# Performance work log

Measured on AMD Instinct MI355X. Metric: run time of the kernel, lower is better.

The kernel has to match this reference:

```python
import jax, jax.numpy as jnp
import numpy as np

D_EMBED = 1024
D_HEAD = 128


def setup_inputs() -> dict:
    key = jax.random.key(0)
    kx, kq, kk, kv = jax.random.split(key, 4)
    x = jax.random.normal(kx, (4, 4096, D_EMBED), dtype=jnp.float32)
    # nn.Linear(d_embed, d_head, bias=False) weights, stored [out, in] like torch
    s = 1.0 / np.sqrt(D_EMBED)
    Wq = jax.random.uniform(kq, (D_HEAD, D_EMBED), jnp.float32, -s, s)
    Wk = jax.random.uniform(kk, (D_HEAD, D_EMBED), jnp.float32, -s, s)
    Wv = jax.random.uniform(kv, (D_HEAD, D_EMBED), jnp.float32, -s, s)
    return {"x": x, "Wq": Wq, "Wk": Wk, "Wv": Wv}


def reference(x, Wq, Wk, Wv):
    # q,k,v: [b, s, d_head]
    q = jnp.einsum("bse,he->bsh", x, Wq)
    k = jnp.einsum("bse,he->bsh", x, Wk)
    v = jnp.einsum("bse,he->bsh", x, Wv)
    # original: (q @ k^T) * d_head**-0.5, then divided by sqrt(d_embed)
    scale = 1.0 / (np.sqrt(D_HEAD) * np.sqrt(D_EMBED))
    scores = jnp.einsum("bqh,bkh->bqk", q, k) * jnp.float32(scale)  # [b, s, s]
    attn = jax.nn.softmax(scores, axis=-1)
    return jnp.einsum("bqk,bkh->bqh", attn, v)
```

## Files before the change

kernel.cpp:

```cpp
#include <hip/hip_runtime.h>
#include <stdint.h>

typedef __bf16 bf16x8 __attribute__((ext_vector_type(8)));
typedef float  f32x4  __attribute__((ext_vector_type(4)));

#define ATTN_SCALE 2.7621359e-3f

__device__ __forceinline__ unsigned short f2bf(float f) {
  union { float f; uint32_t u; } v; v.f = f;
  uint32_t u = v.u;
  uint32_t r = (u + 0x7FFFu + ((u >> 16) & 1u)) >> 16;
  return (unsigned short)r;
}

__device__ __forceinline__ void load_lds16(const unsigned short* g, unsigned short* l) {
  __builtin_amdgcn_global_load_lds(
      (const __attribute__((address_space(1))) void*)g,
      (__attribute__((address_space(3))) void*)l, 16, 0, 0);
}

__device__ __forceinline__ f32x4 mfma16(bf16x8 a, bf16x8 b, f32x4 c) {
  return __builtin_amdgcn_mfma_f32_16x16x32_bf16(a, b, c, 0, 0, 0);
}

__device__ __forceinline__ bf16x8 ones_bf16() {
  union { unsigned short u[8]; bf16x8 v; } c;
#pragma unroll
  for (int j = 0; j < 8; ++j) c.u[j] = 0x3F80;
  return c.v;
}

__global__ __launch_bounds__(256) void k_cvt(const float* __restrict__ src,
                                             unsigned short* __restrict__ dst, int n4) {
  int i = blockIdx.x * 256 + threadIdx.x;
  if (i >= n4) return;
  float4 f = ((const float4*)src)[i];
  ushort4 o;
  o.x = f2bf(f.x); o.y = f2bf(f.y); o.z = f2bf(f.z); o.w = f2bf(f.w);
  ((ushort4*)dst)[i] = o;
}

__global__ __launch_bounds__(256) void k_cvtw(const float* __restrict__ a,
                                              const float* __restrict__ b,
                                              const float* __restrict__ c,
                                              unsigned short* __restrict__ dst) {
  int i = blockIdx.x * 256 + threadIdx.x;
  int sel = i >> 15, off = i & 32767;
  const float* s = (sel == 0) ? a : (sel == 1) ? b : c;
  float4 f = ((const float4*)s)[off];
  ushort4 o;
  o.x = f2bf(f.x); o.y = f2bf(f.y); o.z = f2bf(f.z); o.w = f2bf(f.w);
  ((ushort4*)dst)[i] = o;
}

__global__ __launch_bounds__(256, 2) void k_proj(
    const unsigned short* __restrict__ X,
    const unsigned short* __restrict__ W,
    unsigned short* __restrict__ Qb,
    unsigned short* __restrict__ Kb,
    unsigned short* __restrict__ Vt)
{
  __shared__ __align__(16) unsigned short sm[128 * 32 * 2];
  unsigned short* As = sm;
  unsigned short* Bs = sm + 4096;
  const int t = threadIdx.x;
  const int mtile = blockIdx.x;
  const int nt = blockIdx.y;
  const int w = t >> 6, lane = t & 63, quad = lane >> 4, l15 = lane & 15;
  const int wm = w & 1, wn = w >> 1;

  const unsigned short* Wsel = W + nt * (128 * 1024);
  const unsigned short* Ag = X + (size_t)(mtile * 128) * 1024;

  const unsigned short* ag0 = Ag + (size_t)(t >> 2) * 1024 + (t & 3) * 8;
  const unsigned short* bg0 = Wsel + (size_t)(t >> 2) * 1024 + (t & 3) * 8;
  unsigned short* aw = &As[(t >> 6) * 512];
  unsigned short* bw = &Bs[(t >> 6) * 512];

  f32x4 acc[4][4] = {};

  for (int kt = 0; kt < 32; ++kt) {
    __syncthreads();
    const unsigned short* ak = ag0 + kt * 32;
    const unsigned short* bk = bg0 + kt * 32;
    load_lds16(ak,             aw);
    load_lds16(ak + 64 * 1024, aw + 2048);
    load_lds16(bk,             bw);
    load_lds16(bk + 64 * 1024, bw + 2048);
    __syncthreads();

    bf16x8 af[4], bfr[4];
#pragma unroll
    for (int i = 0; i < 4; ++i)
      af[i] = *(const bf16x8*)&As[(wm * 64 + i * 16 + l15) * 32 + quad * 8];
#pragma unroll
    for (int j = 0; j < 4; ++j)
      bfr[j] = *(const bf16x8*)&Bs[(wn * 64 + j * 16 + l15) * 32 + quad * 8];
#pragma unroll
    for (int i = 0; i < 4; ++i)
#pragma unroll
      for (int j = 0; j < 4; ++j)
        acc[i][j] = mfma16(af[i], bfr[j], acc[i][j]);
  }

  if (nt != 2) {
    const int m0 = mtile * 128 + wm * 64;
#pragma unroll
    for (int i = 0; i < 4; ++i)
#pragma unroll
      for (int j = 0; j < 4; ++j)
#pragma unroll
        for (int r = 0; r < 4; ++r) {
          int m = m0 + i * 16 + quad * 4 + r;
          int n = wn * 64 + j * 16 + l15;
          float v = acc[i][j][r];
          if (nt == 0) Qb[(size_t)m * 128 + n] = f2bf(v * ATTN_SCALE);
          else         Kb[(size_t)m * 128 + n] = f2bf(v);
        }
  } else {
    float* Ts = (float*)sm;
    const int bb = mtile >> 5;
    const int s0 = (mtile & 31) * 128;
#pragma unroll
    for (int jj = 0; jj < 8; ++jj) {
      __syncthreads();
      if (wn == (jj >> 2)) {
        const int j = jj & 3;
#pragma unroll
        for (int i = 0; i < 4; ++i)
#pragma unroll
          for (int r = 0; r < 4; ++r)
            Ts[(wm * 64 + i * 16 + quad * 4 + r) * 17 + l15] = acc[i][j][r];
      }
      __syncthreads();
      int n2 = jj * 16 + (t >> 4), m2 = (t & 15) * 8;
      union { unsigned short u[8]; uint4 v; } pk;
#pragma unroll
      for (int e = 0; e < 8; ++e) pk.u[e] = f2bf(Ts[(m2 + e) * 17 + (t >> 4)]);
      *(uint4*)&Vt[((size_t)(bb * 128 + n2)) * 4096 + s0 + m2] = pk.v;
    }
  }
}

__global__ __launch_bounds__(256, 2) void k_flash(
    const unsigned short* __restrict__ Qb,
    const unsigned short* __restrict__ Kb,
    const unsigned short* __restrict__ Vt,
    float* __restrict__ Om,
    float* __restrict__ lp)
{
  __shared__ __align__(16) unsigned short smem[8192 * 3 + 5120];
  unsigned short* Vsh = smem + 16384;
  unsigned short* Psh = smem + 24576;
  float* Ob  = (float*)smem;
  float* lsh = (float*)(smem + 24576);

  const int t = threadIdx.x;
  const int w = t >> 6, lane = t & 63, quad = lane >> 4, l15 = lane & 15;
  const int h = w & 1, p = w >> 1;
  const int qt = blockIdx.x, b = blockIdx.y, sp = blockIdx.z;

  const unsigned short* Qg = Qb + (size_t)(b * 4096 + qt * 64 + h * 32) * 128;
  const unsigned short* Kg = Kb + (size_t)b * 4096 * 128;
  const unsigned short* Vg = Vt + (size_t)b * 128 * 4096;

  bf16x8 qf[2][4];
#pragma unroll
  for (int mt = 0; mt < 2; ++mt)
#pragma unroll
    for (int kk = 0; kk < 4; ++kk)
      qf[mt][kk] = *(const bf16x8*)&Qg[(size_t)(mt * 16 + l15) * 128 + kk * 32 + quad * 8];

  f32x4 O[2][8] = {};
  f32x4 Ol[2] = {};

  const unsigned short* kg0 = Kg + (size_t)(t >> 4) * 128 + (((t & 15) ^ ((t >> 5) & 7)) * 8);
  const unsigned short* vg0 = Vg + (size_t)(t >> 3) * 4096 + (((t & 7) ^ ((t >> 3) & 7)) * 8);
  unsigned short* vw = &Vsh[w * 512];

  const int kt0 = sp * 32;

  {
    const unsigned short* kg = kg0 + (size_t)kt0 * 8192;
    unsigned short* kw = &smem[w * 512];
#pragma unroll
    for (int it = 0; it < 4; ++it)
      load_lds16(kg + it * 2048, kw + it * 2048);
  }

  for (int i = 0; i < 32; ++i) {
    const int cur = i & 1, nxt = cur ^ 1;
    __syncthreads();
    {
      const unsigned short* vg = vg0 + (size_t)(kt0 + i) * 64;
#pragma unroll
      for (int it = 0; it < 4; ++it)
        load_lds16(vg + (size_t)it * 131072, vw + it * 2048);
      const int ktn = (i < 31) ? (kt0 + i + 1) : kt0;
      const unsigned short* kg = kg0 + (size_t)ktn * 8192;
      unsigned short* kw = &smem[nxt * 8192 + w * 512];
#pragma unroll
      for (int it = 0; it < 4; ++it)
        load_lds16(kg + it * 2048, kw + it * 2048);
    }

    const unsigned short* Kshc = &smem[cur * 8192];
    f32x4 sc[2][2] = {};
#pragma unroll
    for (int ntk = 0; ntk < 2; ++ntk) {
      const int row = p * 32 + 2 * l15 + ntk;
#pragma unroll
      for (int kk = 0; kk < 4; ++kk) {
        bf16x8 kf = *(const bf16x8*)&Kshc[row * 128 + (((kk * 4 + quad) ^ (l15 & 7)) * 8)];
        sc[0][ntk] = mfma16(qf[0][kk], kf, sc[0][ntk]);
        sc[1][ntk] = mfma16(qf[1][kk], kf, sc[1][ntk]);
      }
    }

#pragma unroll
    for (int mt = 0; mt < 2; ++mt)
#pragma unroll
      for (int r = 0; r < 4; ++r) {
        float e0 = __expf(sc[mt][0][r]);
        float e1 = __expf(sc[mt][1][r]);
        int row = mt * 16 + quad * 4 + r;
        uint32_t pk = (uint32_t)f2bf(e0) | ((uint32_t)f2bf(e1) << 16);
        *(uint32_t*)&Psh[w * 1280 + row * 40 + 2 * l15] = pk;
      }

    asm volatile("s_waitcnt vmcnt(4) lgkmcnt(0)" ::: "memory");
    asm volatile("s_barrier" ::: "memory");

    bf16x8 pf0 = *(const bf16x8*)&Psh[w * 1280 + l15 * 40 + quad * 8];
    bf16x8 pf1 = *(const bf16x8*)&Psh[w * 1280 + (16 + l15) * 40 + quad * 8];
    const bf16x8 one = ones_bf16();
    Ol[0] = mfma16(pf0, one, Ol[0]);
    Ol[1] = mfma16(pf1, one, Ol[1]);
#pragma unroll
    for (int dt = 0; dt < 8; ++dt) {
      bf16x8 vf = *(const bf16x8*)&Vsh[(dt * 16 + l15) * 64 + (((p * 4 + quad) ^ (l15 & 7)) * 8)];
      O[0][dt] = mfma16(pf0, vf, O[0][dt]);
      O[1][dt] = mfma16(pf1, vf, O[1][dt]);
    }
  }

  __syncthreads();
  if (p == 1) {
#pragma unroll
    for (int mt = 0; mt < 2; ++mt)
#pragma unroll
      for (int r = 0; r < 4; ++r) {
        int row = h * 32 + mt * 16 + quad * 4 + r;
        if (l15 == 0) lsh[row] = Ol[mt][r];
#pragma unroll
        for (int dt = 0; dt < 8; ++dt)
          Ob[row * 128 + dt * 16 + l15] = O[mt][dt][r];
      }
  }
  __syncthreads();
  if (p == 0) {
    const size_t rowbase = (size_t)b * 4096 + qt * 64;
    float* Omp = Om + (size_t)sp * 2097152;
#pragma unroll
    for (int mt = 0; mt < 2; ++mt)
#pragma unroll
      for (int r = 0; r < 4; ++r) {
        int row = h * 32 + mt * 16 + quad * 4 + r;
#pragma unroll
        for (int dt = 0; dt < 8; ++dt)
          Omp[(rowbase + row) * 128 + dt * 16 + l15] =
              O[mt][dt][r] + Ob[row * 128 + dt * 16 + l15];
        if (l15 == 0)
          lp[(size_t)sp * 16384 + rowbase + row] = Ol[mt][r] + lsh[row];
      }
  }
}

__global__ __launch_bounds__(256) void k_merge(const float* __restrict__ Om,
                                               const float* __restrict__ lp,
                                               float* __restrict__ out) {
  int i = blockIdx.x * 256 + threadIdx.x;
  int row = i >> 5;
  float inv = 1.0f / (lp[row] + lp[16384 + row]);
  float4 a = ((const float4*)Om)[i];
  float4 c = ((const float4*)Om)[524288 + i];
  float4 o;
  o.x = (a.x + c.x) * inv;
  o.y = (a.y + c.y) * inv;
  o.z = (a.z + c.z) * inv;
  o.w = (a.w + c.w) * inv;
  ((float4*)out)[i] = o;
}

extern "C" void kernel_launch(void* const* d_in, const int* in_sizes, int n_in,
                              void* d_out, int out_size, void* d_ws, size_t ws_size,
                              hipStream_t stream) {
  const float* x  = (const float*)d_in[0];
  const float* Wq = (const float*)d_in[1];
  const float* Wk = (const float*)d_in[2];
  const float* Wv = (const float*)d_in[3];
  float* out = (float*)d_out;

  unsigned short* ws  = (unsigned short*)d_ws;
  unsigned short* xbf = ws;
  unsigned short* wbf = xbf + 16777216;
  unsigned short* Qb  = wbf + 393216;
  unsigned short* Kb  = Qb + 2097152;
  unsigned short* Vt  = Kb + 2097152;
  float* lp  = (float*)(Vt + 2097152);
  float* Om  = (float*)xbf;

  k_cvt<<<16384, 256, 0, stream>>>(x, xbf, 4194304);
  k_cvtw<<<384, 256, 0, stream>>>(Wq, Wk, Wv, wbf);
  k_proj<<<dim3(128, 3), 256, 0, stream>>>(xbf, wbf, Qb, Kb, Vt);
  k_flash<<<dim3(64, 4, 2), 256, 0, stream>>>(Qb, Kb, Vt, Om, lp);
  k_merge<<<2048, 256, 0, stream>>>(Om, lp, out);
}
```

Before: 180.0 us.

## Split flash attention KV range four ways, drop K double-buffer to raise occupancy

Splits the key range across four blocks instead of two, doubling the grid. The K tile is single-buffered, which cuts shared memory so three blocks can fit per CU, and the P scratch stride is tightened. The merge kernel now sums four partial outputs and normalizers. The cost is lost K prefetch overlap, an extra wait and barrier per iteration, and double the partial-output traffic, which needs Om to fit four partial slices in the workspace.

Result: slower. 188.5 us (+4.7%).

```diff
diff --git a/kernel.cpp b/kernel.cpp
--- a/kernel.cpp
+++ b/kernel.cpp
@@ -142,18 +142,18 @@
   }
 }
 
-__global__ __launch_bounds__(256, 2) void k_flash(
+__global__ __launch_bounds__(256, 3) void k_flash(
     const unsigned short* __restrict__ Qb,
     const unsigned short* __restrict__ Kb,
     const unsigned short* __restrict__ Vt,
     float* __restrict__ Om,
     float* __restrict__ lp)
 {
-  __shared__ __align__(16) unsigned short smem[8192 * 3 + 5120];
-  unsigned short* Vsh = smem + 16384;
-  unsigned short* Psh = smem + 24576;
+  __shared__ __align__(16) unsigned short smem[20480];
+  unsigned short* Vsh = smem + 8192;
+  unsigned short* Psh = smem + 16384;
   float* Ob  = (float*)smem;
-  float* lsh = (float*)(smem + 24576);
+  float* lsh = (float*)(smem + 16384);
 
   const int t = threadIdx.x;
   const int w = t >> 6, lane = t & 63, quad = lane >> 4, l15 = lane & 15;
@@ -176,42 +176,33 @@
 
   const unsigned short* kg0 = Kg + (size_t)(t >> 4) * 128 + (((t & 15) ^ ((t >> 5) & 7)) * 8);
   const unsigned short* vg0 = Vg + (size_t)(t >> 3) * 4096 + (((t & 7) ^ ((t >> 3) & 7)) * 8);
+  unsigned short* kw = &smem[w * 512];
   unsigned short* vw = &Vsh[w * 512];
 
-  const int kt0 = sp * 32;
-
-  {
-    const unsigned short* kg = kg0 + (size_t)kt0 * 8192;
-    unsigned short* kw = &smem[w * 512];
-#pragma unroll
-    for (int it = 0; it < 4; ++it)
-      load_lds16(kg + it * 2048, kw + it * 2048);
-  }
-
-  for (int i = 0; i < 32; ++i) {
-    const int cur = i & 1, nxt = cur ^ 1;
+  const int kt0 = sp * 16;
+
+  for (int i = 0; i < 16; ++i) {
     __syncthreads();
     {
+      const unsigned short* kg = kg0 + (size_t)(kt0 + i) * 8192;
+#pragma unroll
+      for (int it = 0; it < 4; ++it)
+        load_lds16(kg + it * 2048, kw + it * 2048);
       const unsigned short* vg = vg0 + (size_t)(kt0 + i) * 64;
 #pragma unroll
       for (int it = 0; it < 4; ++it)
         load_lds16(vg + (size_t)it * 131072, vw + it * 2048);
-      const int ktn = (i < 31) ? (kt0 + i + 1) : kt0;
-      const unsigned short* kg = kg0 + (size_t)ktn * 8192;
-      unsigned short* kw = &smem[nxt * 8192 + w * 512];
-#pragma unroll
-      for (int it = 0; it < 4; ++it)
-        load_lds16(kg + it * 2048, kw + it * 2048);
     }
-
-    const unsigned short* Kshc = &smem[cur * 8192];
+    asm volatile("s_waitcnt vmcnt(4)" ::: "memory");
+    asm volatile("s_barrier" ::: "memory");
+
     f32x4 sc[2][2] = {};
 #pragma unroll
     for (int ntk = 0; ntk < 2; ++ntk) {
       const int row = p * 32 + 2 * l15 + ntk;
 #pragma unroll
       for (int kk = 0; kk < 4; ++kk) {
-        bf16x8 kf = *(const bf16x8*)&Kshc[row * 128 + (((kk * 4 + quad) ^ (l15 & 7)) * 8)];
+        bf16x8 kf = *(const bf16x8*)&smem[row * 128 + (((kk * 4 + quad) ^ (l15 & 7)) * 8)];
         sc[0][ntk] = mfma16(qf[0][kk], kf, sc[0][ntk]);
         sc[1][ntk] = mfma16(qf[1][kk], kf, sc[1][ntk]);
       }
@@ -224,15 +215,15 @@
         float e0 = __expf(sc[mt][0][r]);
         float e1 = __expf(sc[mt][1][r]);
         int row = mt * 16 + quad * 4 + r;
-        uint32_t pk = (uint32_t)f2bf(e0) | ((uint32_t)f2bf(e1) << 16);
-        *(uint32_t*)&Psh[w * 1280 + row * 40 + 2 * l15] = pk;
-      }
-
-    asm volatile("s_waitcnt vmcnt(4) lgkmcnt(0)" ::: "memory");
+        uint32_t pkv = (uint32_t)f2bf(e0) | ((uint32_t)f2bf(e1) << 16);
+        *(uint32_t*)&Psh[w * 1024 + row * 32 + 2 * l15] = pkv;
+      }
+
+    asm volatile("s_waitcnt vmcnt(0) lgkmcnt(0)" ::: "memory");
     asm volatile("s_barrier" ::: "memory");
 
-    bf16x8 pf0 = *(const bf16x8*)&Psh[w * 1280 + l15 * 40 + quad * 8];
-    bf16x8 pf1 = *(const bf16x8*)&Psh[w * 1280 + (16 + l15) * 40 + quad * 8];
+    bf16x8 pf0 = *(const bf16x8*)&Psh[w * 1024 + l15 * 32 + quad * 8];
+    bf16x8 pf1 = *(const bf16x8*)&Psh[w * 1024 + (16 + l15) * 32 + quad * 8];
     const bf16x8 one = ones_bf16();
     Ol[0] = mfma16(pf0, one, Ol[0]);
     Ol[1] = mfma16(pf1, one, Ol[1]);
@@ -281,14 +272,16 @@
                                                float* __restrict__ out) {
   int i = blockIdx.x * 256 + threadIdx.x;
   int row = i >> 5;
-  float inv = 1.0f / (lp[row] + lp[16384 + row]);
+  float inv = 1.0f / (lp[row] + lp[16384 + row] + lp[32768 + row] + lp[49152 + row]);
   float4 a = ((const float4*)Om)[i];
   float4 c = ((const float4*)Om)[524288 + i];
+  float4 d = ((const float4*)Om)[1048576 + i];
+  float4 e = ((const float4*)Om)[1572864 + i];
   float4 o;
-  o.x = (a.x + c.x) * inv;
-  o.y = (a.y + c.y) * inv;
-  o.z = (a.z + c.z) * inv;
-  o.w = (a.w + c.w) * inv;
+  o.x = (a.x + c.x + d.x + e.x) * inv;
+  o.y = (a.y + c.y + d.y + e.y) * inv;
+  o.z = (a.z + c.z + d.z + e.z) * inv;
+  o.w = (a.w + c.w + d.w + e.w) * inv;
   ((float4*)out)[i] = o;
 }
 
@@ -313,6 +306,6 @@
   k_cvt<<<16384, 256, 0, stream>>>(x, xbf, 4194304);
   k_cvtw<<<384, 256, 0, stream>>>(Wq, Wk, Wv, wbf);
   k_proj<<<dim3(128, 3), 256, 0, stream>>>(xbf, wbf, Qb, Kb, Vt);
-  k_flash<<<dim3(64, 4, 2), 256, 0, stream>>>(Qb, Kb, Vt, Om, lp);
+  k_flash<<<dim3(64, 4, 4), 256, 0, stream>>>(Qb, Kb, Vt, Om, lp);
   k_merge<<<2048, 256, 0, stream>>>(Om, lp, out);
 }
```

## Fuse fp32-to-bf16 conversion into projection and double-buffer V in flash kernel

Applied to the files above, without the earlier changes.

The separate conversion kernels for x and the weights are removed. The projection kernel now loads fp32 directly, converts to bf16 in registers, and writes to LDS, with a register prefetch of the next k-tile. This avoids writing and re-reading a bf16 copy of x, a large tensor. A new flash variant double-buffers both K and V in LDS using dynamic shared memory of about 74 KB, which drops the mid-iteration barrier. It falls back to the old single-buffered kernel if the attribute call fails. The larger LDS footprint may reduce occupancy below two blocks per CU.

Measured after the change: 181.3 us. Within noise of the previous version (+0.7%).

```diff
diff --git a/kernel.cpp b/kernel.cpp
--- a/kernel.cpp
+++ b/kernel.cpp
@@ -30,32 +30,11 @@
   return c.v;
 }
 
-__global__ __launch_bounds__(256) void k_cvt(const float* __restrict__ src,
-                                             unsigned short* __restrict__ dst, int n4) {
-  int i = blockIdx.x * 256 + threadIdx.x;
-  if (i >= n4) return;
-  float4 f = ((const float4*)src)[i];
-  ushort4 o;
-  o.x = f2bf(f.x); o.y = f2bf(f.y); o.z = f2bf(f.z); o.w = f2bf(f.w);
-  ((ushort4*)dst)[i] = o;
-}
-
-__global__ __launch_bounds__(256) void k_cvtw(const float* __restrict__ a,
-                                              const float* __restrict__ b,
-                                              const float* __restrict__ c,
-                                              unsigned short* __restrict__ dst) {
-  int i = blockIdx.x * 256 + threadIdx.x;
-  int sel = i >> 15, off = i & 32767;
-  const float* s = (sel == 0) ? a : (sel == 1) ? b : c;
-  float4 f = ((const float4*)s)[off];
-  ushort4 o;
-  o.x = f2bf(f.x); o.y = f2bf(f.y); o.z = f2bf(f.z); o.w = f2bf(f.w);
-  ((ushort4*)dst)[i] = o;
-}
-
 __global__ __launch_bounds__(256, 2) void k_proj(
-    const unsigned short* __restrict__ X,
-    const unsigned short* __restrict__ W,
+    const float* __restrict__ Xf,
+    const float* __restrict__ Wqf,
+    const float* __restrict__ Wkf,
+    const float* __restrict__ Wvf,
     unsigned short* __restrict__ Qb,
     unsigned short* __restrict__ Kb,
     unsigned short* __restrict__ Vt)
@@ -69,25 +48,44 @@
   const int w = t >> 6, lane = t & 63, quad = lane >> 4, l15 = lane & 15;
   const int wm = w & 1, wn = w >> 1;
 
-  const unsigned short* Wsel = W + nt * (128 * 1024);
-  const unsigned short* Ag = X + (size_t)(mtile * 128) * 1024;
-
-  const unsigned short* ag0 = Ag + (size_t)(t >> 2) * 1024 + (t & 3) * 8;
-  const unsigned short* bg0 = Wsel + (size_t)(t >> 2) * 1024 + (t & 3) * 8;
-  unsigned short* aw = &As[(t >> 6) * 512];
-  unsigned short* bw = &Bs[(t >> 6) * 512];
+  const float* Wsel = (nt == 0) ? Wqf : (nt == 1) ? Wkf : Wvf;
+  const int srow = t >> 1;
+  const int scol = (t & 1) * 16;
+  const float* ax = Xf + ((size_t)(mtile * 128 + srow)) * 1024 + scol;
+  const float* bx = Wsel + (size_t)srow * 1024 + scol;
+  unsigned short* adst = &As[srow * 32 + scol];
+  unsigned short* bdst = &Bs[srow * 32 + scol];
 
   f32x4 acc[4][4] = {};
 
+  float4 ar[4], br[4];
+#pragma unroll
+  for (int j = 0; j < 4; ++j) {
+    ar[j] = *(const float4*)(ax + 4 * j);
+    br[j] = *(const float4*)(bx + 4 * j);
+  }
+
   for (int kt = 0; kt < 32; ++kt) {
-    __syncthreads();
-    const unsigned short* ak = ag0 + kt * 32;
-    const unsigned short* bk = bg0 + kt * 32;
-    load_lds16(ak,             aw);
-    load_lds16(ak + 64 * 1024, aw + 2048);
-    load_lds16(bk,             bw);
-    load_lds16(bk + 64 * 1024, bw + 2048);
-    __syncthreads();
+    union { unsigned short u[16]; uint4 v[2]; } pa, pb;
+#pragma unroll
+    for (int j = 0; j < 4; ++j) {
+      pa.u[4 * j]     = f2bf(ar[j].x); pa.u[4 * j + 1] = f2bf(ar[j].y);
+      pa.u[4 * j + 2] = f2bf(ar[j].z); pa.u[4 * j + 3] = f2bf(ar[j].w);
+      pb.u[4 * j]     = f2bf(br[j].x); pb.u[4 * j + 1] = f2bf(br[j].y);
+      pb.u[4 * j + 2] = f2bf(br[j].z); pb.u[4 * j + 3] = f2bf(br[j].w);
+    }
+    *(uint4*)adst = pa.v[0]; *(uint4*)(adst + 8) = pa.v[1];
+    *(uint4*)bdst = pb.v[0]; *(uint4*)(bdst + 8) = pb.v[1];
+
+    const int ktn = (kt < 31) ? kt + 1 : 31;
+#pragma unroll
+    for (int j = 0; j < 4; ++j) {
+      ar[j] = *(const float4*)(ax + ktn * 32 + 4 * j);
+      br[j] = *(const float4*)(bx + ktn * 32 + 4 * j);
+    }
+
+    asm volatile("s_waitcnt lgkmcnt(0)" ::: "memory");
+    asm volatile("s_barrier" ::: "memory");
 
     bf16x8 af[4], bfr[4];
 #pragma unroll
@@ -101,6 +99,8 @@
 #pragma unroll
       for (int j = 0; j < 4; ++j)
         acc[i][j] = mfma16(af[i], bfr[j], acc[i][j]);
+
+    asm volatile("s_barrier" ::: "memory");
   }
 
   if (nt != 2) {
@@ -142,7 +142,141 @@
   }
 }
 
-__global__ __launch_bounds__(256, 2) void k_flash(
+__global__ __launch_bounds__(256, 2) void k_flash_db(
+    const unsigned short* __restrict__ Qb,
+    const unsigned short* __restrict__ Kb,
+    const unsigned short* __restrict__ Vt,
+    float* __restrict__ Om,
+    float* __restrict__ lp)
+{
+  extern __shared__ __align__(16) unsigned short sm[];
+  unsigned short* Psh = sm + 32768;
+  float* Ob  = (float*)sm;
+  float* lsh = (float*)(sm + 32768);
+
+  const int t = threadIdx.x;
+  const int w = t >> 6, lane = t & 63, quad = lane >> 4, l15 = lane & 15;
+  const int h = w & 1, p = w >> 1;
+  const int qt = blockIdx.x, b = blockIdx.y, sp = blockIdx.z;
+
+  const unsigned short* Qg = Qb + (size_t)(b * 4096 + qt * 64 + h * 32) * 128;
+  const unsigned short* Kg = Kb + (size_t)b * 4096 * 128;
+  const unsigned short* Vg = Vt + (size_t)b * 128 * 4096;
+
+  bf16x8 qf[2][4];
+#pragma unroll
+  for (int mt = 0; mt < 2; ++mt)
+#pragma unroll
+    for (int kk = 0; kk < 4; ++kk)
+      qf[mt][kk] = *(const bf16x8*)&Qg[(size_t)(mt * 16 + l15) * 128 + kk * 32 + quad * 8];
+
+  f32x4 O[2][8] = {};
+  f32x4 Ol[2] = {};
+
+  const unsigned short* kg0 = Kg + (size_t)(t >> 4) * 128 + (((t & 15) ^ ((t >> 5) & 7)) * 8);
+  const unsigned short* vg0 = Vg + (size_t)(t >> 3) * 4096 + (((t & 7) ^ ((t >> 3) & 7)) * 8);
+
+  const int kt0 = sp * 32;
+
+  {
+    const unsigned short* kg = kg0 + (size_t)kt0 * 8192;
+    const unsigned short* vg = vg0 + (size_t)kt0 * 64;
+    unsigned short* kw = sm + w * 512;
+    unsigned short* vw = sm + 16384 + w * 512;
+#pragma unroll
+    for (int it = 0; it < 4; ++it) load_lds16(kg + it * 2048, kw + it * 2048);
+#pragma unroll
+    for (int it = 0; it < 4; ++it) load_lds16(vg + (size_t)it * 131072, vw + it * 2048);
+  }
+
+  for (int i = 0; i < 32; ++i) {
+    const int cur = i & 1, nxt = cur ^ 1;
+    __syncthreads();
+
+    {
+      const int ktn = (i < 31) ? (kt0 + i + 1) : kt0;
+      const unsigned short* kg = kg0 + (size_t)ktn * 8192;
+      const unsigned short* vg = vg0 + (size_t)ktn * 64;
+      unsigned short* kw = sm + nxt * 8192 + w * 512;
+      unsigned short* vw = sm + 16384 + nxt * 8192 + w * 512;
+#pragma unroll
+      for (int it = 0; it < 4; ++it) load_lds16(kg + it * 2048, kw + it * 2048);
+#pragma unroll
+      for (int it = 0; it < 4; ++it) load_lds16(vg + (size_t)it * 131072, vw + it * 2048);
+    }
+
+    const unsigned short* Kc = sm + cur * 8192;
+    f32x4 sc[2][2] = {};
+#pragma unroll
+    for (int ntk = 0; ntk < 2; ++ntk) {
+      const int row = p * 32 + 2 * l15 + ntk;
+#pragma unroll
+      for (int kk = 0; kk < 4; ++kk) {
+        bf16x8 kf = *(const bf16x8*)&Kc[row * 128 + (((kk * 4 + quad) ^ (l15 & 7)) * 8)];
+        sc[0][ntk] = mfma16(qf[0][kk], kf, sc[0][ntk]);
+        sc[1][ntk] = mfma16(qf[1][kk], kf, sc[1][ntk]);
+      }
+    }
+
+#pragma unroll
+    for (int mt = 0; mt < 2; ++mt)
+#pragma unroll
+      for (int r = 0; r < 4; ++r) {
+        float e0 = __expf(sc[mt][0][r]);
+        float e1 = __expf(sc[mt][1][r]);
+        int row = mt * 16 + quad * 4 + r;
+        uint32_t pkv = (uint32_t)f2bf(e0) | ((uint32_t)f2bf(e1) << 16);
+        *(uint32_t*)&Psh[w * 1280 + row * 40 + 2 * l15] = pkv;
+      }
+    asm volatile("s_waitcnt lgkmcnt(0)" ::: "memory");
+
+    const unsigned short* Vc = sm + 16384 + cur * 8192;
+    bf16x8 pf0 = *(const bf16x8*)&Psh[w * 1280 + l15 * 40 + quad * 8];
+    bf16x8 pf1 = *(const bf16x8*)&Psh[w * 1280 + (16 + l15) * 40 + quad * 8];
+    const bf16x8 one = ones_bf16();
+    Ol[0] = mfma16(pf0, one, Ol[0]);
+    Ol[1] = mfma16(pf1, one, Ol[1]);
+#pragma unroll
+    for (int dt = 0; dt < 8; ++dt) {
+      bf16x8 vf = *(const bf16x8*)&Vc[(dt * 16 + l15) * 64 + (((p * 4 + quad) ^ (l15 & 7)) * 8)];
+      O[0][dt] = mfma16(pf0, vf, O[0][dt]);
+      O[1][dt] = mfma16(pf1, vf, O[1][dt]);
+    }
+  }
+
+  __syncthreads();
+  if (p == 1) {
+#pragma unroll
+    for (int mt = 0; mt < 2; ++mt)
+#pragma unroll
+      for (int r = 0; r < 4; ++r) {
+        int row = h * 32 + mt * 16 + quad * 4 + r;
+        if (l15 == 0) lsh[row] = Ol[mt][r];
+#pragma unroll
+        for (int dt = 0; dt < 8; ++dt)
+          Ob[row * 128 + dt * 16 + l15] = O[mt][dt][r];
+      }
+  }
+  __syncthreads();
+  if (p == 0) {
+    const size_t rowbase = (size_t)b * 4096 + qt * 64;
+    float* Omp = Om + (size_t)sp * 2097152;
+#pragma unroll
+    for (int mt = 0; mt < 2; ++mt)
+#pragma unroll
+      for (int r = 0; r < 4; ++r) {
+        int row = h * 32 + mt * 16 + quad * 4 + r;
+#pragma unroll
+        for (int dt = 0; dt < 8; ++dt)
+          Omp[(rowbase + row) * 128 + dt * 16 + l15] =
+              O[mt][dt][r] + Ob[row * 128 + dt * 16 + l15];
+        if (l15 == 0)
+          lp[(size_t)sp * 16384 + rowbase + row] = Ol[mt][r] + lsh[row];
+      }
+  }
+}
+
+__global__ __launch_bounds__(256, 2) void k_flash_sb(
     const unsigned short* __restrict__ Qb,
     const unsigned short* __restrict__ Kb,
     const unsigned short* __restrict__ Vt,
@@ -179,13 +313,11 @@
   unsigned short* vw = &Vsh[w * 512];
 
   const int kt0 = sp * 32;
-
   {
     const unsigned short* kg = kg0 + (size_t)kt0 * 8192;
     unsigned short* kw = &smem[w * 512];
 #pragma unroll
-    for (int it = 0; it < 4; ++it)
-      load_lds16(kg + it * 2048, kw + it * 2048);
+    for (int it = 0; it < 4; ++it) load_lds16(kg + it * 2048, kw + it * 2048);
   }
 
   for (int i = 0; i < 32; ++i) {
@@ -194,14 +326,12 @@
     {
       const unsigned short* vg = vg0 + (size_t)(kt0 + i) * 64;
 #pragma unroll
-      for (int it = 0; it < 4; ++it)
-        load_lds16(vg + (size_t)it * 131072, vw + it * 2048);
+      for (int it = 0; it < 4; ++it) load_lds16(vg + (size_t)it * 131072, vw + it * 2048);
       const int ktn = (i < 31) ? (kt0 + i + 1) : kt0;
       const unsigned short* kg = kg0 + (size_t)ktn * 8192;
       unsigned short* kw = &smem[nxt * 8192 + w * 512];
 #pragma unroll
-      for (int it = 0; it < 4; ++it)
-        load_lds16(kg + it * 2048, kw + it * 2048);
+      for (int it = 0; it < 4; ++it) load_lds16(kg + it * 2048, kw + it * 2048);
     }
 
     const unsigned short* Kshc = &smem[cur * 8192];
@@ -224,8 +354,8 @@
         float e0 = __expf(sc[mt][0][r]);
         float e1 = __expf(sc[mt][1][r]);
         int row = mt * 16 + quad * 4 + r;
-        uint32_t pk = (uint32_t)f2bf(e0) | ((uint32_t)f2bf(e1) << 16);
-        *(uint32_t*)&Psh[w * 1280 + row * 40 + 2 * l15] = pk;
+        uint32_t pkv = (uint32_t)f2bf(e0) | ((uint32_t)f2bf(e1) << 16);
+        *(uint32_t*)&Psh[w * 1280 + row * 40 + 2 * l15] = pkv;
       }
 
     asm volatile("s_waitcnt vmcnt(4) lgkmcnt(0)" ::: "memory");
@@ -301,18 +431,23 @@
   const float* Wv = (const float*)d_in[3];
   float* out = (float*)d_out;
 
-  unsigned short* ws  = (unsigned short*)d_ws;
-  unsigned short* xbf = ws;
-  unsigned short* wbf = xbf + 16777216;
-  unsigned short* Qb  = wbf + 393216;
-  unsigned short* Kb  = Qb + 2097152;
-  unsigned short* Vt  = Kb + 2097152;
-  float* lp  = (float*)(Vt + 2097152);
-  float* Om  = (float*)xbf;
-
-  k_cvt<<<16384, 256, 0, stream>>>(x, xbf, 4194304);
-  k_cvtw<<<384, 256, 0, stream>>>(Wq, Wk, Wv, wbf);
-  k_proj<<<dim3(128, 3), 256, 0, stream>>>(xbf, wbf, Qb, Kb, Vt);
-  k_flash<<<dim3(64, 4, 2), 256, 0, stream>>>(Qb, Kb, Vt, Om, lp);
+  unsigned short* ws = (unsigned short*)d_ws;
+  unsigned short* Qb = ws;
+  unsigned short* Kb = ws + 2097152;
+  unsigned short* Vt = ws + 4194304;
+  float* lp = (float*)(ws + 6291456);
+  float* Om = (float*)(ws + 6356992);
+
+  k_proj<<<dim3(128, 3), 256, 0, stream>>>(x, Wq, Wk, Wv, Qb, Kb, Vt);
+
+  const unsigned int DBU_LDS = 75776;
+  hipError_t e = hipFuncSetAttribute(
+      reinterpret_cast<const void*>(k_flash_db),
+      hipFuncAttributeMaxDynamicSharedMemorySize, DBU_LDS);
+  if (e == hipSuccess) {
+    k_flash_db<<<dim3(64, 4, 2), 256, DBU_LDS, stream>>>(Qb, Kb, Vt, Om, lp);
+  } else {
+    k_flash_sb<<<dim3(64, 4, 2), 256, 0, stream>>>(Qb, Kb, Vt, Om, lp);
+  }
   k_merge<<<2048, 256, 0, stream>>>(Om, lp, out);
 }
```
